# Performance work log

Measured on AMD Instinct MI355X. Metric: run time of the kernel, lower is better.

## Reference

```python
import jax, jax.numpy as jnp
import numpy as np

U, I, D = 50000, 25000, 128          # users, items, emb_size
E = 1_000_000                        # user-item interactions
L = 3                                # num_layers
B = 4096                             # BPR batch size
N = U + I                            # total graph nodes


def setup_inputs() -> dict:
    key = jax.random.key(0)
    k1, k2, k3, k4, k5, k6, k7 = jax.random.split(key, 7)
    # Xavier-ish embedding tables
    user_emb = jax.random.normal(k1, (U, D), jnp.float32) * 0.1
    item_emb = jax.random.normal(k2, (I, D), jnp.float32) * 0.1
    # random bipartite interactions -> symmetric COO adjacency over N nodes
    eu = jax.random.randint(k3, (E,), 0, U)            # user node ids
    ei = jax.random.randint(k4, (E,), 0, I) + U        # item node ids (offset)
    adj_row = jnp.concatenate([eu, ei]).astype(jnp.int32)   # [2E]
    adj_col = jnp.concatenate([ei, eu]).astype(jnp.int32)   # [2E]
    # symmetric normalization D^-1/2 A D^-1/2 (matches create_adj_mat)
    deg = jax.ops.segment_sum(jnp.ones(2 * E, jnp.float32), adj_row, num_segments=N)
    d_inv = jnp.where(deg > 0, deg ** -0.5, 0.0)
    adj_vals = d_inv[adj_row] * d_inv[adj_col]               # [2E] float32
    users = jax.random.randint(k5, (B,), 0, U).astype(jnp.int32)
    pos_items = jax.random.randint(k6, (B,), 0, I).astype(jnp.int32)
    neg_items = jax.random.randint(k7, (B,), 0, I).astype(jnp.int32)
    return dict(user_emb=user_emb, item_emb=item_emb, adj_row=adj_row,
                adj_col=adj_col, adj_vals=adj_vals, users=users,
                pos_items=pos_items, neg_items=neg_items)


def _spmm(vals, row, col, x):
    # sparse [N,N] @ dense [N,D] via gather + segment_sum
    return jax.ops.segment_sum(vals[:, None] * x[col], row, num_segments=N)


def reference(user_emb, item_emb, adj_row, adj_col, adj_vals,
              users, pos_items, neg_items):
    ego = jnp.concatenate([user_emb, item_emb], axis=0)      # [N, D]
    # FAITHFUL to the torch source: ego_embeddings is never reassigned inside
    # the layer loop, so every one of the L layer outputs equals A @ ego.
    # mean(stack([ego, A@ego, ..., A@ego])) == (ego + L * A@ego) / (L + 1)
    h = _spmm(adj_vals, adj_row, adj_col, ego)               # [N, D]
    final = (ego + L * h) / (L + 1)                          # mean over L+1 layers
    u_final = final[:U]
    i_final = final[U:]
    u_g = u_final[users]                                     # [B, D]
    pos_i_g = i_final[pos_items]                             # [B, D]
    neg_i_g = i_final[neg_items]                             # [B, D]
    return (u_g, pos_i_g, neg_i_g, i_final)
```

## Files before the change

### kernel.cpp

```cpp
#include <hip/hip_runtime.h>
#include <hip/hip_bf16.h>

#define U_CNT 50000
#define I_CNT 25000
#define D_DIM 128
#define E_CNT 1000000
#define B_CNT 4096
#define ICAP 96
#define UCAP 64
#define BM_WORDS 1600


__device__ __forceinline__ unsigned pack_bf2(float lo, float hi) {
    __hip_bfloat16 a = __float2bfloat16(lo);
    __hip_bfloat16 b = __float2bfloat16(hi);
    unsigned short ua = *reinterpret_cast<unsigned short*>(&a);
    unsigned short ub = *reinterpret_cast<unsigned short*>(&b);
    return ((unsigned)ub << 16) | ua;
}
__device__ __forceinline__ float bf_lo(unsigned w) { return __uint_as_float(w << 16); }
__device__ __forceinline__ float bf_hi(unsigned w) { return __uint_as_float(w & 0xffff0000u); }

__global__ void rep_kernel(const int* __restrict__ users,
                           unsigned* __restrict__ bitmap,
                           int* __restrict__ slot) {
    int j = blockIdx.x * blockDim.x + threadIdx.x;
    if (j >= B_CNT) return;
    const int u = users[j];
    atomicOr(&bitmap[u >> 5], 1u << (u & 31));
    atomicCAS(&slot[u], 0, j + 1);
}

__global__ __launch_bounds__(256) void cvt_kernel(
        const float* __restrict__ src, unsigned* __restrict__ dst, int n_dw) {
    int i = blockIdx.x * blockDim.x + threadIdx.x;
    if (i >= n_dw) return;
    float2 f = ((const float2*)src)[i];
    dst[i] = pack_bf2(f.x, f.y);
}

__global__ __launch_bounds__(256) void bucket_kernel(
        const int*      __restrict__ adj_row,
        const int*      __restrict__ adj_col,
        const float*    __restrict__ adj_vals,
        const unsigned* __restrict__ bitmap,
        const int*      __restrict__ slot,
        int*  __restrict__ icnt,  int*  __restrict__ ucnt,
        int2* __restrict__ ibuck, int2* __restrict__ ubuck) {
    const int base = (blockIdx.x * blockDim.x + threadIdx.x) * 4;
    if (base >= E_CNT) return;
    const int4   uu = *(const int4*)  (adj_row  + base);
    const int4   tt = *(const int4*)  (adj_col  + base);
    const float4 vv = *(const float4*)(adj_vals + base);

    const int   us[4] = {uu.x, uu.y, uu.z, uu.w};
    const int   ts[4] = {tt.x - U_CNT, tt.y - U_CNT, tt.z - U_CNT, tt.w - U_CNT};
    const float vs[4] = {vv.x, vv.y, vv.z, vv.w};

#pragma unroll
    for (int k = 0; k < 4; ++k) {
        const int u = us[k], t = ts[k];
        const int vb = __float_as_int(vs[k]);
        const int c = atomicAdd(&icnt[t], 1);
        ibuck[(size_t)t * ICAP + c] = make_int2(u, vb);
        if ((bitmap[u >> 5] >> (u & 31)) & 1u) {
            const int j0 = slot[u] - 1;
            const int c2 = atomicAdd(&ucnt[j0], 1);
            ubuck[(size_t)j0 * UCAP + c2] = make_int2(t, vb);
        }
    }
}

__global__ __launch_bounds__(256) void item_gather_kernel(
        const float*    __restrict__ item_emb,
        const unsigned* __restrict__ ue16,
        const int*      __restrict__ icnt,
        const int2*     __restrict__ ibuck,
        float*          __restrict__ out) {
    const int lane = threadIdx.x & 63;
    const int t    = (blockIdx.x * blockDim.x + threadIdx.x) >> 6;
    if (t >= I_CNT) return;

    const int   n = icnt[t];
    const int2* b = ibuck + (size_t)t * ICAP;
    float ax = 0.0f, ay = 0.0f;

    int p = 0;
    for (; p + 4 <= n; p += 4) {
        const int2 e0 = b[p], e1 = b[p + 1], e2 = b[p + 2], e3 = b[p + 3];
        const unsigned w0 = ue16[(size_t)e0.x * 64 + lane];
        const unsigned w1 = ue16[(size_t)e1.x * 64 + lane];
        const unsigned w2 = ue16[(size_t)e2.x * 64 + lane];
        const unsigned w3 = ue16[(size_t)e3.x * 64 + lane];
        const float v0 = __int_as_float(e0.y), v1 = __int_as_float(e1.y);
        const float v2 = __int_as_float(e2.y), v3 = __int_as_float(e3.y);
        ax += v0 * bf_lo(w0) + v1 * bf_lo(w1) + v2 * bf_lo(w2) + v3 * bf_lo(w3);
        ay += v0 * bf_hi(w0) + v1 * bf_hi(w1) + v2 * bf_hi(w2) + v3 * bf_hi(w3);
    }
    for (; p < n; ++p) {
        const int2 e = b[p];
        const unsigned w = ue16[(size_t)e.x * 64 + lane];
        const float v = __int_as_float(e.y);
        ax += v * bf_lo(w);
        ay += v * bf_hi(w);
    }

    const float2 eg = ((const float2*)(item_emb + (size_t)t * D_DIM))[lane];
    float2 o;
    o.x = (eg.x + 3.0f * ax) * 0.25f;
    o.y = (eg.y + 3.0f * ay) * 0.25f;
    ((float2*)(out + (size_t)(3 * B_CNT + t) * D_DIM))[lane] = o;
}

__global__ __launch_bounds__(256) void user_gather_kernel(
        const float* __restrict__ user_emb,
        const float* __restrict__ item_emb,
        const int*   __restrict__ users,
        const int*   __restrict__ slot,
        const int*   __restrict__ ucnt,
        const int2*  __restrict__ ubuck,
        float*       __restrict__ out) {
    const int lane = threadIdx.x & 63;
    const int j    = (blockIdx.x * blockDim.x + threadIdx.x) >> 6;
    if (j >= B_CNT) return;
    const int u = users[j];
    if (slot[u] - 1 != j) return;

    const int   n = ucnt[j];
    const int2* b = ubuck + (size_t)j * UCAP;
    float ax = 0.0f, ay = 0.0f;

    int p = 0;
    for (; p + 4 <= n; p += 4) {
        const int2 e0 = b[p], e1 = b[p + 1], e2 = b[p + 2], e3 = b[p + 3];
        const float2 x0 = ((const float2*)(item_emb + (size_t)e0.x * D_DIM))[lane];
        const float2 x1 = ((const float2*)(item_emb + (size_t)e1.x * D_DIM))[lane];
        const float2 x2 = ((const float2*)(item_emb + (size_t)e2.x * D_DIM))[lane];
        const float2 x3 = ((const float2*)(item_emb + (size_t)e3.x * D_DIM))[lane];
        const float v0 = __int_as_float(e0.y), v1 = __int_as_float(e1.y);
        const float v2 = __int_as_float(e2.y), v3 = __int_as_float(e3.y);
        ax += v0 * x0.x + v1 * x1.x + v2 * x2.x + v3 * x3.x;
        ay += v0 * x0.y + v1 * x1.y + v2 * x2.y + v3 * x3.y;
    }
    for (; p < n; ++p) {
        const int2 e = b[p];
        const float2 x = ((const float2*)(item_emb + (size_t)e.x * D_DIM))[lane];
        const float v = __int_as_float(e.y);
        ax += v * x.x;
        ay += v * x.y;
    }

    const float2 eg = ((const float2*)(user_emb + (size_t)u * D_DIM))[lane];
    float2 o;
    o.x = (eg.x + 3.0f * ax) * 0.25f;
    o.y = (eg.y + 3.0f * ay) * 0.25f;
    ((float2*)(out + (size_t)j * D_DIM))[lane] = o;
}

__global__ __launch_bounds__(256) void finalize_kernel(
        const int* __restrict__ users,
        const int* __restrict__ slot,
        const int* __restrict__ pos_items,
        const int* __restrict__ neg_items,
        float*     __restrict__ out) {
    const int lane = threadIdx.x & 63;
    const int w    = (blockIdx.x * blockDim.x + threadIdx.x) >> 6;
    if (w >= 3 * B_CNT) return;

    if (w < B_CNT) {
        const int u  = users[w];
        const int j0 = slot[u] - 1;
        if (j0 == w) return;
        const float2 v = ((const float2*)(out + (size_t)j0 * D_DIM))[lane];
        ((float2*)(out + (size_t)w * D_DIM))[lane] = v;
    } else {
        const int q   = w - B_CNT;
        const int idx = (q < B_CNT) ? pos_items[q] : neg_items[q - B_CNT];
        const float2 v = ((const float2*)(out + (size_t)(3 * B_CNT + idx) * D_DIM))[lane];
        ((float2*)(out + (size_t)w * D_DIM))[lane] = v;
    }
}

extern "C" void kernel_launch(void* const* d_in, const int* in_sizes, int n_in,
                              void* d_out, int out_size, void* d_ws, size_t ws_size,
                              hipStream_t stream) {
    const float* user_emb  = (const float*)d_in[0];
    const float* item_emb  = (const float*)d_in[1];
    const int*   adj_row   = (const int*)  d_in[2];
    const int*   adj_col   = (const int*)  d_in[3];
    const float* adj_vals  = (const float*)d_in[4];
    const int*   users     = (const int*)  d_in[5];
    const int*   pos_items = (const int*)  d_in[6];
    const int*   neg_items = (const int*)  d_in[7];
    float* out = (float*)d_out;

    unsigned* bitmap = (unsigned*)d_ws;
    int* slot = (int*)(bitmap + BM_WORDS);
    int* icnt = slot + U_CNT;
    int* ucnt = icnt + I_CNT;
    int2* ibuck = (int2*)(ucnt + B_CNT);
    int2* ubuck = ibuck + (size_t)I_CNT * ICAP;
    unsigned* ue16 = (unsigned*)(ubuck + (size_t)B_CNT * UCAP);

    hipMemsetAsync(bitmap, 0,
                   (size_t)(BM_WORDS + U_CNT + I_CNT + B_CNT) * sizeof(int),
                   stream);

    rep_kernel<<<(B_CNT + 255) / 256, 256, 0, stream>>>(users, bitmap, slot);

    cvt_kernel<<<(U_CNT * 64 + 255) / 256, 256, 0, stream>>>(
        user_emb, ue16, U_CNT * 64);

    bucket_kernel<<<(E_CNT / 4 + 255) / 256, 256, 0, stream>>>(
        adj_row, adj_col, adj_vals, bitmap, slot, icnt, ucnt, ibuck, ubuck);

    item_gather_kernel<<<(I_CNT * 64 + 255) / 256, 256, 0, stream>>>(
        item_emb, ue16, icnt, ibuck, out);

    user_gather_kernel<<<(B_CNT * 64 + 255) / 256, 256, 0, stream>>>(
        user_emb, item_emb, users, slot, ucnt, ubuck, out);

    finalize_kernel<<<(3 * B_CNT * 64 + 255) / 256, 256, 0, stream>>>(
        users, slot, pos_items, neg_items, out);
}
```

Measured before the change: 230.8 us.

## Fuse all stages into one cooperative persistent kernel with XCD-partitioned bucketing

Replaces the memset and six separate launches with a single cooperative kernel that runs every stage and separates them with grid-wide syncs. It removes per-launch overhead and the idle gaps between the small kernels. It also splits the edge bucketing by blockIdx&7 so each group of blocks handles only one eighth of the item and user ranges, which is meant to keep atomics and bucket writes local to one XCD's L2. The costs are that each edge is read by all 8 block groups, the grid is fixed at 1024 blocks with lower parallelism in the gather phases, and grid.sync adds barrier overhead.

```diff
diff --git a/kernel.cpp b/kernel.cpp
--- a/kernel.cpp
+++ b/kernel.cpp
@@ -1,5 +1,8 @@
 #include <hip/hip_runtime.h>
 #include <hip/hip_bf16.h>
+#include <hip/hip_cooperative_groups.h>
+
+namespace cg = cooperative_groups;
 
 #define U_CNT 50000
 #define I_CNT 25000
@@ -9,6 +12,15 @@
 #define ICAP 96
 #define UCAP 64
 #define BM_WORDS 1600
+#define ZERO_INTS (BM_WORDS + U_CNT + I_CNT + B_CNT)
+
+#define NBLK 1024
+#define NTHR 256
+#define NWAVES (NBLK * 4)
+#define IRANGE (I_CNT / 8)
+#define URANGE (U_CNT / 8)
+#define NGRP (NBLK / 8)
+#define CHUNK 7816
 
 
 __device__ __forceinline__ unsigned pack_bf2(float lo, float hi) {
@@ -21,163 +33,161 @@
 __device__ __forceinline__ float bf_lo(unsigned w) { return __uint_as_float(w << 16); }
 __device__ __forceinline__ float bf_hi(unsigned w) { return __uint_as_float(w & 0xffff0000u); }
 
-__global__ void rep_kernel(const int* __restrict__ users,
-                           unsigned* __restrict__ bitmap,
-                           int* __restrict__ slot) {
-    int j = blockIdx.x * blockDim.x + threadIdx.x;
-    if (j >= B_CNT) return;
-    const int u = users[j];
-    atomicOr(&bitmap[u >> 5], 1u << (u & 31));
-    atomicCAS(&slot[u], 0, j + 1);
-}
-
-__global__ __launch_bounds__(256) void cvt_kernel(
-        const float* __restrict__ src, unsigned* __restrict__ dst, int n_dw) {
-    int i = blockIdx.x * blockDim.x + threadIdx.x;
-    if (i >= n_dw) return;
-    float2 f = ((const float2*)src)[i];
-    dst[i] = pack_bf2(f.x, f.y);
-}
-
-__global__ __launch_bounds__(256) void bucket_kernel(
-        const int*      __restrict__ adj_row,
-        const int*      __restrict__ adj_col,
-        const float*    __restrict__ adj_vals,
-        const unsigned* __restrict__ bitmap,
-        const int*      __restrict__ slot,
-        int*  __restrict__ icnt,  int*  __restrict__ ucnt,
-        int2* __restrict__ ibuck, int2* __restrict__ ubuck) {
-    const int base = (blockIdx.x * blockDim.x + threadIdx.x) * 4;
-    if (base >= E_CNT) return;
-    const int4   uu = *(const int4*)  (adj_row  + base);
-    const int4   tt = *(const int4*)  (adj_col  + base);
-    const float4 vv = *(const float4*)(adj_vals + base);
-
-    const int   us[4] = {uu.x, uu.y, uu.z, uu.w};
-    const int   ts[4] = {tt.x - U_CNT, tt.y - U_CNT, tt.z - U_CNT, tt.w - U_CNT};
-    const float vs[4] = {vv.x, vv.y, vv.z, vv.w};
-
-#pragma unroll
-    for (int k = 0; k < 4; ++k) {
-        const int u = us[k], t = ts[k];
-        const int vb = __float_as_int(vs[k]);
-        const int c = atomicAdd(&icnt[t], 1);
-        ibuck[(size_t)t * ICAP + c] = make_int2(u, vb);
-        if ((bitmap[u >> 5] >> (u & 31)) & 1u) {
-            const int j0 = slot[u] - 1;
-            const int c2 = atomicAdd(&ucnt[j0], 1);
-            ubuck[(size_t)j0 * UCAP + c2] = make_int2(t, vb);
-        }
-    }
-}
-
-__global__ __launch_bounds__(256) void item_gather_kernel(
-        const float*    __restrict__ item_emb,
-        const unsigned* __restrict__ ue16,
-        const int*      __restrict__ icnt,
-        const int2*     __restrict__ ibuck,
-        float*          __restrict__ out) {
-    const int lane = threadIdx.x & 63;
-    const int t    = (blockIdx.x * blockDim.x + threadIdx.x) >> 6;
-    if (t >= I_CNT) return;
-
-    const int   n = icnt[t];
-    const int2* b = ibuck + (size_t)t * ICAP;
-    float ax = 0.0f, ay = 0.0f;
-
-    int p = 0;
-    for (; p + 4 <= n; p += 4) {
-        const int2 e0 = b[p], e1 = b[p + 1], e2 = b[p + 2], e3 = b[p + 3];
-        const unsigned w0 = ue16[(size_t)e0.x * 64 + lane];
-        const unsigned w1 = ue16[(size_t)e1.x * 64 + lane];
-        const unsigned w2 = ue16[(size_t)e2.x * 64 + lane];
-        const unsigned w3 = ue16[(size_t)e3.x * 64 + lane];
-        const float v0 = __int_as_float(e0.y), v1 = __int_as_float(e1.y);
-        const float v2 = __int_as_float(e2.y), v3 = __int_as_float(e3.y);
-        ax += v0 * bf_lo(w0) + v1 * bf_lo(w1) + v2 * bf_lo(w2) + v3 * bf_lo(w3);
-        ay += v0 * bf_hi(w0) + v1 * bf_hi(w1) + v2 * bf_hi(w2) + v3 * bf_hi(w3);
-    }
-    for (; p < n; ++p) {
-        const int2 e = b[p];
-        const unsigned w = ue16[(size_t)e.x * 64 + lane];
-        const float v = __int_as_float(e.y);
-        ax += v * bf_lo(w);
-        ay += v * bf_hi(w);
-    }
-
-    const float2 eg = ((const float2*)(item_emb + (size_t)t * D_DIM))[lane];
-    float2 o;
-    o.x = (eg.x + 3.0f * ax) * 0.25f;
-    o.y = (eg.y + 3.0f * ay) * 0.25f;
-    ((float2*)(out + (size_t)(3 * B_CNT + t) * D_DIM))[lane] = o;
-}
-
-__global__ __launch_bounds__(256) void user_gather_kernel(
+__global__ __launch_bounds__(NTHR) void mega_kernel(
         const float* __restrict__ user_emb,
         const float* __restrict__ item_emb,
+        const int*   __restrict__ adj_row,
+        const int*   __restrict__ adj_col,
+        const float* __restrict__ adj_vals,
         const int*   __restrict__ users,
-        const int*   __restrict__ slot,
-        const int*   __restrict__ ucnt,
-        const int2*  __restrict__ ubuck,
+        const int*   __restrict__ pos_items,
+        const int*   __restrict__ neg_items,
+        unsigned*    __restrict__ bitmap,
+        int*         __restrict__ slot,
+        int*         __restrict__ icnt,
+        int*         __restrict__ ucnt,
+        int2*        __restrict__ ibuck,
+        int2*        __restrict__ ubuck,
+        unsigned*    __restrict__ ue16,
         float*       __restrict__ out) {
+    cg::grid_group grid = cg::this_grid();
+    const int tid  = blockIdx.x * NTHR + threadIdx.x;
+    const int nthr = NBLK * NTHR;
     const int lane = threadIdx.x & 63;
-    const int j    = (blockIdx.x * blockDim.x + threadIdx.x) >> 6;
-    if (j >= B_CNT) return;
-    const int u = users[j];
-    if (slot[u] - 1 != j) return;
-
-    const int   n = ucnt[j];
-    const int2* b = ubuck + (size_t)j * UCAP;
-    float ax = 0.0f, ay = 0.0f;
-
-    int p = 0;
-    for (; p + 4 <= n; p += 4) {
-        const int2 e0 = b[p], e1 = b[p + 1], e2 = b[p + 2], e3 = b[p + 3];
-        const float2 x0 = ((const float2*)(item_emb + (size_t)e0.x * D_DIM))[lane];
-        const float2 x1 = ((const float2*)(item_emb + (size_t)e1.x * D_DIM))[lane];
-        const float2 x2 = ((const float2*)(item_emb + (size_t)e2.x * D_DIM))[lane];
-        const float2 x3 = ((const float2*)(item_emb + (size_t)e3.x * D_DIM))[lane];
-        const float v0 = __int_as_float(e0.y), v1 = __int_as_float(e1.y);
-        const float v2 = __int_as_float(e2.y), v3 = __int_as_float(e3.y);
-        ax += v0 * x0.x + v1 * x1.x + v2 * x2.x + v3 * x3.x;
-        ay += v0 * x0.y + v1 * x1.y + v2 * x2.y + v3 * x3.y;
-    }
-    for (; p < n; ++p) {
-        const int2 e = b[p];
-        const float2 x = ((const float2*)(item_emb + (size_t)e.x * D_DIM))[lane];
-        const float v = __int_as_float(e.y);
-        ax += v * x.x;
-        ay += v * x.y;
-    }
-
-    const float2 eg = ((const float2*)(user_emb + (size_t)u * D_DIM))[lane];
-    float2 o;
-    o.x = (eg.x + 3.0f * ax) * 0.25f;
-    o.y = (eg.y + 3.0f * ay) * 0.25f;
-    ((float2*)(out + (size_t)j * D_DIM))[lane] = o;
-}
-
-__global__ __launch_bounds__(256) void finalize_kernel(
-        const int* __restrict__ users,
-        const int* __restrict__ slot,
-        const int* __restrict__ pos_items,
-        const int* __restrict__ neg_items,
-        float*     __restrict__ out) {
-    const int lane = threadIdx.x & 63;
-    const int w    = (blockIdx.x * blockDim.x + threadIdx.x) >> 6;
-    if (w >= 3 * B_CNT) return;
-
-    if (w < B_CNT) {
-        const int u  = users[w];
-        const int j0 = slot[u] - 1;
-        if (j0 == w) return;
-        const float2 v = ((const float2*)(out + (size_t)j0 * D_DIM))[lane];
-        ((float2*)(out + (size_t)w * D_DIM))[lane] = v;
-    } else {
-        const int q   = w - B_CNT;
-        const int idx = (q < B_CNT) ? pos_items[q] : neg_items[q - B_CNT];
-        const float2 v = ((const float2*)(out + (size_t)(3 * B_CNT + idx) * D_DIM))[lane];
-        ((float2*)(out + (size_t)w * D_DIM))[lane] = v;
+    const int wib  = threadIdx.x >> 6;
+
+    for (int i = tid; i < ZERO_INTS; i += nthr) ((int*)bitmap)[i] = 0;
+    for (int i = tid; i < U_CNT * 64; i += nthr) {
+        const float2 f = ((const float2*)user_emb)[i];
+        ue16[i] = pack_bf2(f.x, f.y);
+    }
+    grid.sync();
+
+    if (tid < B_CNT) {
+        const int u = users[tid];
+        atomicOr(&bitmap[u >> 5], 1u << (u & 31));
+        atomicCAS(&slot[u], 0, tid + 1);
+    }
+    grid.sync();
+
+    {
+        const unsigned x = blockIdx.x & 7;
+        const int g      = blockIdx.x >> 3;
+        const int start  = g * CHUNK;
+        const int end    = min(E_CNT, start + CHUNK);
+        for (int e = start + (int)threadIdx.x * 4; e < end; e += NTHR * 4) {
+            const int4   uu = *(const int4*)  (adj_row  + e);
+            const int4   tt = *(const int4*)  (adj_col  + e);
+            const float4 vv = *(const float4*)(adj_vals + e);
+            const unsigned us[4] = {(unsigned)uu.x, (unsigned)uu.y,
+                                    (unsigned)uu.z, (unsigned)uu.w};
+            const unsigned ts[4] = {(unsigned)(tt.x - U_CNT), (unsigned)(tt.y - U_CNT),
+                                    (unsigned)(tt.z - U_CNT), (unsigned)(tt.w - U_CNT)};
+            const float    vs[4] = {vv.x, vv.y, vv.z, vv.w};
+#pragma unroll
+            for (int k = 0; k < 4; ++k) {
+                const unsigned u = us[k], t = ts[k];
+                const int vb = __float_as_int(vs[k]);
+                if (t / IRANGE == x) {
+                    const int c = atomicAdd(&icnt[t], 1);
+                    ibuck[(size_t)t * ICAP + c] = make_int2((int)u, vb);
+                }
+                if (u / URANGE == x) {
+                    if ((bitmap[u >> 5] >> (u & 31)) & 1u) {
+                        const int j0 = slot[u] - 1;
+                        const int c2 = atomicAdd(&ucnt[j0], 1);
+                        ubuck[(size_t)j0 * UCAP + c2] = make_int2((int)t, vb);
+                    }
+                }
+            }
+        }
+    }
+    grid.sync();
+
+    {
+        const int x  = blockIdx.x & 7;
+        const int g  = blockIdx.x >> 3;
+        const int lw = g * 4 + wib;
+        for (int idx = lw; idx < IRANGE; idx += NGRP * 4) {
+            const int t = x * IRANGE + idx;
+            const int   n = icnt[t];
+            const int2* b = ibuck + (size_t)t * ICAP;
+            float ax = 0.0f, ay = 0.0f;
+            int p = 0;
+            for (; p + 4 <= n; p += 4) {
+                const int2 e0 = b[p], e1 = b[p+1], e2 = b[p+2], e3 = b[p+3];
+                const unsigned w0 = ue16[(size_t)e0.x * 64 + lane];
+                const unsigned w1 = ue16[(size_t)e1.x * 64 + lane];
+                const unsigned w2 = ue16[(size_t)e2.x * 64 + lane];
+                const unsigned w3 = ue16[(size_t)e3.x * 64 + lane];
+                const float v0 = __int_as_float(e0.y), v1 = __int_as_float(e1.y);
+                const float v2 = __int_as_float(e2.y), v3 = __int_as_float(e3.y);
+                ax += v0*bf_lo(w0) + v1*bf_lo(w1) + v2*bf_lo(w2) + v3*bf_lo(w3);
+                ay += v0*bf_hi(w0) + v1*bf_hi(w1) + v2*bf_hi(w2) + v3*bf_hi(w3);
+            }
+            for (; p < n; ++p) {
+                const int2 e = b[p];
+                const unsigned w = ue16[(size_t)e.x * 64 + lane];
+                const float v = __int_as_float(e.y);
+                ax += v * bf_lo(w);
+                ay += v * bf_hi(w);
+            }
+            const float2 eg = ((const float2*)(item_emb + (size_t)t * D_DIM))[lane];
+            float2 o;
+            o.x = (eg.x + 3.0f * ax) * 0.25f;
+            o.y = (eg.y + 3.0f * ay) * 0.25f;
+            ((float2*)(out + (size_t)(3 * B_CNT + t) * D_DIM))[lane] = o;
+        }
+
+        const int j = blockIdx.x * 4 + wib;
+        if (j < B_CNT) {
+            const int u = users[j];
+            if (slot[u] - 1 == j) {
+                const int   n = ucnt[j];
+                const int2* b = ubuck + (size_t)j * UCAP;
+                float ax = 0.0f, ay = 0.0f;
+                int p = 0;
+                for (; p + 4 <= n; p += 4) {
+                    const int2 e0 = b[p], e1 = b[p+1], e2 = b[p+2], e3 = b[p+3];
+                    const float2 x0 = ((const float2*)(item_emb + (size_t)e0.x * D_DIM))[lane];
+                    const float2 x1 = ((const float2*)(item_emb + (size_t)e1.x * D_DIM))[lane];
+                    const float2 x2 = ((const float2*)(item_emb + (size_t)e2.x * D_DIM))[lane];
+                    const float2 x3 = ((const float2*)(item_emb + (size_t)e3.x * D_DIM))[lane];
+                    const float v0 = __int_as_float(e0.y), v1 = __int_as_float(e1.y);
+                    const float v2 = __int_as_float(e2.y), v3 = __int_as_float(e3.y);
+                    ax += v0*x0.x + v1*x1.x + v2*x2.x + v3*x3.x;
+                    ay += v0*x0.y + v1*x1.y + v2*x2.y + v3*x3.y;
+                }
+                for (; p < n; ++p) {
+                    const int2 e = b[p];
+                    const float2 xx = ((const float2*)(item_emb + (size_t)e.x * D_DIM))[lane];
+                    const float v = __int_as_float(e.y);
+                    ax += v * xx.x;
+                    ay += v * xx.y;
+                }
+                const float2 eg = ((const float2*)(user_emb + (size_t)u * D_DIM))[lane];
+                float2 o;
+                o.x = (eg.x + 3.0f * ax) * 0.25f;
+                o.y = (eg.y + 3.0f * ay) * 0.25f;
+                ((float2*)(out + (size_t)j * D_DIM))[lane] = o;
+            }
+        }
+    }
+    grid.sync();
+
+    for (int w = blockIdx.x * 4 + wib; w < 3 * B_CNT; w += NWAVES) {
+        if (w < B_CNT) {
+            const int u  = users[w];
+            const int j0 = slot[u] - 1;
+            if (j0 == w) continue;
+            const float2 v = ((const float2*)(out + (size_t)j0 * D_DIM))[lane];
+            ((float2*)(out + (size_t)w * D_DIM))[lane] = v;
+        } else {
+            const int q   = w - B_CNT;
+            const int idx = (q < B_CNT) ? pos_items[q] : neg_items[q - B_CNT];
+            const float2 v = ((const float2*)(out + (size_t)(3 * B_CNT + idx) * D_DIM))[lane];
+            ((float2*)(out + (size_t)w * D_DIM))[lane] = v;
+        }
     }
 }
 
@@ -202,24 +212,12 @@
     int2* ubuck = ibuck + (size_t)I_CNT * ICAP;
     unsigned* ue16 = (unsigned*)(ubuck + (size_t)B_CNT * UCAP);
 
-    hipMemsetAsync(bitmap, 0,
-                   (size_t)(BM_WORDS + U_CNT + I_CNT + B_CNT) * sizeof(int),
-                   stream);
-
-    rep_kernel<<<(B_CNT + 255) / 256, 256, 0, stream>>>(users, bitmap, slot);
-
-    cvt_kernel<<<(U_CNT * 64 + 255) / 256, 256, 0, stream>>>(
-        user_emb, ue16, U_CNT * 64);
-
-    bucket_kernel<<<(E_CNT / 4 + 255) / 256, 256, 0, stream>>>(
-        adj_row, adj_col, adj_vals, bitmap, slot, icnt, ucnt, ibuck, ubuck);
-
-    item_gather_kernel<<<(I_CNT * 64 + 255) / 256, 256, 0, stream>>>(
-        item_emb, ue16, icnt, ibuck, out);
-
-    user_gather_kernel<<<(B_CNT * 64 + 255) / 256, 256, 0, stream>>>(
-        user_emb, item_emb, users, slot, ucnt, ubuck, out);
-
-    finalize_kernel<<<(3 * B_CNT * 64 + 255) / 256, 256, 0, stream>>>(
-        users, slot, pos_items, neg_items, out);
+    void* args[] = {
+        (void*)&user_emb, (void*)&item_emb, (void*)&adj_row, (void*)&adj_col,
+        (void*)&adj_vals, (void*)&users, (void*)&pos_items, (void*)&neg_items,
+        (void*)&bitmap, (void*)&slot, (void*)&icnt, (void*)&ucnt,
+        (void*)&ibuck, (void*)&ubuck, (void*)&ue16, (void*)&out,
+    };
+    hipLaunchCooperativeKernel((const void*)mega_kernel, dim3(NBLK), dim3(NTHR),
+                               args, 0, stream);
 }
```

Measured after the change: 675.6 us. 193% more time.
